# Performance work log

Hardware: AMD Instinct MI355X
Metric: run time of the kernel (lower is better)

The kernel has to match this reference:

```python
import jax, jax.numpy as jnp
import numpy as np

N = 100000   # num_nodes
E = 3200000  # num_edges
F = 7        # node_features
H = 128      # hidden_dim
D = 64       # embedding_dim
EPS = 1e-5


def setup_inputs() -> dict:
    key = jax.random.key(0)
    ks = jax.random.split(key, 32)
    inp = {}
    inp["x"] = jax.random.normal(ks[0], (N, F), jnp.float32)
    inp["edge_index"] = jax.random.randint(ks[1], (2, E), 0, N, dtype=jnp.int64)
    # input projection
    inp["W_in"] = jax.random.normal(ks[2], (F, H), jnp.float32) * 0.1
    inp["b_in"] = jax.random.normal(ks[3], (H,), jnp.float32) * 0.01
    # 3 GCN layers: 128->128, 128->128, 128->64, each with eval-mode BatchNorm params
    dims = [(H, H), (H, H), (H, D)]
    for i, (di, do) in enumerate(dims):
        k = jax.random.split(ks[4 + i], 6)
        inp[f"W{i}"] = jax.random.normal(k[0], (di, do), jnp.float32) * (1.0 / np.sqrt(di))
        inp[f"b{i}"] = jax.random.normal(k[1], (do,), jnp.float32) * 0.01
        inp[f"g{i}"] = 1.0 + 0.1 * jax.random.normal(k[2], (do,), jnp.float32)
        inp[f"be{i}"] = 0.1 * jax.random.normal(k[3], (do,), jnp.float32)
        inp[f"m{i}"] = 0.1 * jax.random.normal(k[4], (do,), jnp.float32)
        inp[f"v{i}"] = jax.random.uniform(k[5], (do,), jnp.float32, 0.5, 1.5)
    return inp


def _gcn_conv(x, W, b, src, dst, dinv):
    h = x @ W                                   # [N, do]
    coef = dinv[src] * dinv[dst]                # [E]
    agg = jax.ops.segment_sum(h[src] * coef[:, None], dst, num_segments=N)
    # self-loop contribution: norm = dinv[i]^2
    return agg + h * (dinv * dinv)[:, None] + b


def _bn_eval(x, g, be, m, v):
    return (x - m) * (g * jax.lax.rsqrt(v + EPS)) + be


def reference(x, edge_index, W_in, b_in,
              W0, b0, g0, be0, m0, v0,
              W1, b1, g1, be1, m1, v1,
              W2, b2, g2, be2, m2, v2):
    src, dst = edge_index[0], edge_index[1]
    # in-degree with self-loops (same for all layers)
    deg = jax.ops.segment_sum(jnp.ones((E,), x.dtype), dst, num_segments=N) + 1.0
    dinv = jax.lax.rsqrt(deg)

    h = jax.nn.relu(x @ W_in + b_in)            # [N, H]

    # layer 0: conv -> bn -> relu -> (dropout=id, eval) -> residual
    h0 = _gcn_conv(h, W0, b0, src, dst, dinv)
    h0 = jax.nn.relu(_bn_eval(h0, g0, be0, m0, v0)) + h
    # layer 1
    h1 = _gcn_conv(h0, W1, b1, src, dst, dinv)
    h1 = jax.nn.relu(_bn_eval(h1, g1, be1, m1, v1)) + h0
    # layer 2 (final): conv -> bn only (shape changes to D, no residual/relu)
    h2 = _gcn_conv(h1, W2, b2, src, dst, dinv)
    return _bn_eval(h2, g2, be2, m2, v2)        # [N, D]
```

## Files before the change

### kernel.cpp

```cpp
#include <hip/hip_runtime.h>


#define NN 100000
#define NE 3200000
#define FI 7
#define HD 128
#define DD 64
#define EPS 1e-5f
#define NB 196
#define EPB 8192
#define NBLK ((NE + EPB - 1) / EPB)
#define EMAX 20000

typedef float float2v __attribute__((ext_vector_type(2)));
typedef short short8 __attribute__((ext_vector_type(8)));
typedef float f32x4 __attribute__((ext_vector_type(4)));
typedef unsigned uintv4 __attribute__((ext_vector_type(4)));

__device__ __forceinline__ unsigned char f2fp8(float f) {
    return (unsigned char)(__builtin_amdgcn_cvt_pk_fp8_f32(f, f, 0, false) & 0xFF);
}
__device__ __forceinline__ unsigned short f2bf(float f) {
    unsigned u = __float_as_uint(f);
    u += 0x7FFF + ((u >> 16) & 1);
    return (unsigned short)(u >> 16);
}
__device__ __forceinline__ float bf2f(unsigned short s) {
    return __uint_as_float((unsigned)s << 16);
}


__global__ __launch_bounds__(256) void pA_bin(const int* __restrict__ ei,
                                              int* __restrict__ bcnt,
                                              int* __restrict__ ebin) {
    __shared__ int rec[EPB];
    __shared__ unsigned char bk[EPB];
    __shared__ int ls[256];
    __shared__ int cur[NB];
    __shared__ int gb[NB];
    const int t = threadIdx.x;
    const int base = blockIdx.x * EPB;
    const int cnt = min(EPB, NE - base);
    __shared__ int hc[256];
    hc[t] = 0;
    __syncthreads();
    for (int i = t; i < cnt; i += 256)
        atomicAdd(&hc[ei[NE + base + i] >> 9], 1);
    __syncthreads();
    const int myc = hc[t];
    if (t < NB) gb[t] = (myc ? atomicAdd(&bcnt[t], myc) : 0) + t * EMAX;
    ls[t] = myc;
    __syncthreads();
    for (int off = 1; off < 256; off <<= 1) {
        int v = (t >= off) ? ls[t - off] : 0;
        __syncthreads();
        ls[t] += v;
        __syncthreads();
    }
    const int excl = ls[t] - myc;
    __syncthreads();
    ls[t] = excl;
    if (t < NB) cur[t] = excl;
    __syncthreads();
    for (int i = t; i < cnt; i += 256) {
        int s = ei[base + i];
        int d = ei[NE + base + i];
        int b = d >> 9;
        int p = atomicAdd(&cur[b], 1);
        rec[p] = ((d & 511) << 23) | s;
        bk[p] = (unsigned char)b;
    }
    __syncthreads();
    for (int i = t; i < cnt; i += 256) {
        int b = bk[i];
        ebin[gb[b] + (i - ls[b])] = rec[i];
    }
}

__global__ __launch_bounds__(512) void p4_finalize(const int* __restrict__ bcnt,
                                                   const int* __restrict__ ebin,
                                                   int* __restrict__ esrc,
                                                   int* __restrict__ rowstart,
                                                   float* __restrict__ dinv) {
    __shared__ int sh[256];
    __shared__ int lh[512];
    __shared__ int sc[512];
    __shared__ int lc[512];
    const int t = threadIdx.x;
    const int b = blockIdx.x;
    if (t < 256) sh[t] = (t < NB) ? bcnt[t] : 0;
    __syncthreads();
    for (int off = 1; off < 256; off <<= 1) {
        int v = (t < 256 && t >= off) ? sh[t - off] : 0;
        __syncthreads();
        if (t < 256) sh[t] += v;
        __syncthreads();
    }
    const int ecnt = bcnt[b];
    const int ebase = sh[b] - ecnt;
    const int rbase = b * EMAX;
    const int n0 = b << 9;
    lh[t] = 0;
    __syncthreads();
    for (int i = t; i < ecnt; i += 512)
        atomicAdd(&lh[((unsigned)ebin[rbase + i]) >> 23], 1);
    __syncthreads();
    const int c = lh[t];
    sc[t] = c;
    __syncthreads();
    for (int off = 1; off < 512; off <<= 1) {
        int v = (t >= off) ? sc[t - off] : 0;
        __syncthreads();
        sc[t] += v;
        __syncthreads();
    }
    const int excl = ebase + sc[t] - c;
    lc[t] = excl;
    const int node = n0 + t;
    if (node < NN) {
        rowstart[node] = excl;
        dinv[node] = rsqrtf((float)c + 1.0f);
    }
    if (b == NB - 1 && t == 0) rowstart[NN] = NE;
    __syncthreads();
    for (int i = t; i < ecnt; i += 512) {
        int v = ebin[rbase + i];
        int p = atomicAdd(&lc[((unsigned)v) >> 23], 1);
        esrc[p] = v & 0x7FFFFF;
    }
}


__global__ __launch_bounds__(256) void inproj_kernel(const float* __restrict__ x,
                                                     const float* __restrict__ W_in,
                                                     const float* __restrict__ b_in,
                                                     unsigned short* __restrict__ hAbf) {
    int n = blockIdx.x * 2 + (threadIdx.x >> 7);
    int j = threadIdx.x & 127;
    float acc = b_in[j];
#pragma unroll
    for (int f = 0; f < FI; ++f) acc += x[n * FI + f] * W_in[f * HD + j];
    acc = fmaxf(acc, 0.f);
    hAbf[n * HD + j] = f2bf(acc);
}


__global__ __launch_bounds__(64) void wprep_all(const float* __restrict__ W0,
                                                const float* __restrict__ W1,
                                                const float* __restrict__ W2,
                                                unsigned short* __restrict__ wf0,
                                                unsigned short* __restrict__ wf1,
                                                unsigned short* __restrict__ wf2) {
    const int blk = blockIdx.x;
    const float* W;
    unsigned short* Wf;
    int DO, rel;
    if (blk < 32) { W = W0; Wf = wf0; DO = 128; rel = blk; }
    else if (blk < 64) { W = W1; Wf = wf1; DO = 128; rel = blk - 32; }
    else { W = W2; Wf = wf2; DO = 64; rel = blk - 64; }
    const int lane = threadIdx.x;
    const int nt = rel >> 2;
    const int ks = rel & 3;
    short8 o;
#pragma unroll
    for (int j = 0; j < 8; ++j)
        o[j] = (short)f2bf(W[(ks * 32 + (lane >> 4) * 8 + j) * DO + nt * 16 + (lane & 15)]);
    *(short8*)(Wf + ((size_t)rel * 64 + lane) * 8) = o;
}


template <int DO>
__global__ __launch_bounds__(256) void gemm_mfma(const unsigned short* __restrict__ A,
                                                 const unsigned short* __restrict__ Wf,
                                                 const float* __restrict__ dinv,
                                                 unsigned char* __restrict__ B) {
    constexpr int CT = DO / 64;
    const int tid = threadIdx.x;
    const int wave = tid >> 6;
    const int lane = tid & 63;
    const int n0 = blockIdx.x * 32;
    short8 bfrag[CT][4];
#pragma unroll
    for (int ct = 0; ct < CT; ++ct)
#pragma unroll
        for (int ks = 0; ks < 4; ++ks)
            bfrag[ct][ks] = *(const short8*)(Wf + ((size_t)(((wave * CT + ct) * 4 + ks) * 64) + lane) * 8);
#pragma unroll
    for (int rt = 0; rt < 2; ++rt) {
        const int arow = n0 + rt * 16 + (lane & 15);
        short8 afrag[4];
#pragma unroll
        for (int ks = 0; ks < 4; ++ks)
            afrag[ks] = *(const short8*)(A + (size_t)arow * HD + ks * 32 + ((lane >> 4) & 3) * 8);
        f32x4 acc[CT];
#pragma unroll
        for (int ct = 0; ct < CT; ++ct) acc[ct] = (f32x4){0.f, 0.f, 0.f, 0.f};
#pragma unroll
        for (int ks = 0; ks < 4; ++ks)
#pragma unroll
            for (int ct = 0; ct < CT; ++ct)
                acc[ct] = __builtin_amdgcn_mfma_f32_16x16x32_bf16(afrag[ks], bfrag[ct][ks], acc[ct], 0, 0, 0);
#pragma unroll
        for (int r = 0; r < 4; ++r) {
            const int orow = n0 + rt * 16 + (lane >> 4) * 4 + r;
            const float dv = dinv[orow];
#pragma unroll
            for (int ct = 0; ct < CT; ++ct) {
                const int ocol = (wave * CT + ct) * 16 + (lane & 15);
                B[(size_t)orow * DO + ocol] = f2fp8(acc[ct][r] * dv);
            }
        }
    }
}


template <int DO, bool RELU_RES>
__global__ __launch_bounds__(128) void gather_kernel(const unsigned char* __restrict__ hXW,
                                                     float* __restrict__ resOut,
                                                     unsigned short* __restrict__ resBf,
                                                     const int* __restrict__ rowstart,
                                                     const int* __restrict__ esrc,
                                                     const float* __restrict__ dinv,
                                                     const float* __restrict__ bias,
                                                     const float* __restrict__ g,
                                                     const float* __restrict__ be,
                                                     const float* __restrict__ m,
                                                     const float* __restrict__ v) {
    constexpr int CG = DO / 16;
    constexpr int NG = 128 / CG;
    __shared__ int s_idx[128];
    __shared__ float sred[16][132];
    const int n = blockIdx.x;
    const int t = threadIdx.x;
    const int rs = rowstart[n];
    const int re = rowstart[n + 1];
    const float dn = dinv[n];
    const int q = t & (CG - 1);
    const int grp = t / CG;
    float2v aL[4], aH[4], bL[4], bH[4];
#pragma unroll
    for (int w = 0; w < 4; ++w) {
        aL[w] = (float2v){0.f, 0.f}; aH[w] = (float2v){0.f, 0.f};
        bL[w] = (float2v){0.f, 0.f}; bH[w] = (float2v){0.f, 0.f};
    }
    for (int base = rs; base < re; base += 128) {
        const int c = min(128, re - base);
        __syncthreads();
        if (t < c) s_idx[t] = esrc[base + t];
        __syncthreads();
        for (int j = grp; j < c; j += 2 * NG) {
            {
                const uintv4 u = *(const uintv4*)(hXW + (size_t)s_idx[j] * DO + q * 16);
#pragma unroll
                for (int w = 0; w < 4; ++w) {
                    aL[w] += __builtin_amdgcn_cvt_pk_f32_fp8(u[w], false);
                    aH[w] += __builtin_amdgcn_cvt_pk_f32_fp8(u[w], true);
                }
            }
            if (j + NG < c) {
                const uintv4 u = *(const uintv4*)(hXW + (size_t)s_idx[j + NG] * DO + q * 16);
#pragma unroll
                for (int w = 0; w < 4; ++w) {
                    bL[w] += __builtin_amdgcn_cvt_pk_f32_fp8(u[w], false);
                    bH[w] += __builtin_amdgcn_cvt_pk_f32_fp8(u[w], true);
                }
            }
        }
    }
#pragma unroll
    for (int w = 0; w < 4; ++w) { aL[w] += bL[w]; aH[w] += bH[w]; }
#pragma unroll
    for (int w = 0; w < 4; ++w) {
        sred[4 * w + 0][t] = aL[w].x;
        sred[4 * w + 1][t] = aL[w].y;
        sred[4 * w + 2][t] = aH[w].x;
        sred[4 * w + 3][t] = aH[w].y;
    }
    __syncthreads();
    if (t < DO) {
        const int s = t & 15;
        const int q2 = t >> 4;
        float sum = 0.f;
#pragma unroll
        for (int k = 0; k < NG; ++k) sum += sred[s][k * CG + q2];
        const unsigned su = *(const unsigned*)(hXW + (size_t)n * DO + (t & ~3));
        const float2v pLo = __builtin_amdgcn_cvt_pk_f32_fp8(su, false);
        const float2v pHi = __builtin_amdgcn_cvt_pk_f32_fp8(su, true);
        const float slf = (t & 2) ? ((t & 1) ? pHi.y : pHi.x)
                                  : ((t & 1) ? pLo.y : pLo.x);
        float val = (sum + slf) * dn + bias[t];
        val = (val - m[t]) * (g[t] * rsqrtf(v[t] + EPS)) + be[t];
        if (RELU_RES) {
            val = fmaxf(val, 0.f) + bf2f(resBf[(size_t)n * DO + t]);
            resBf[(size_t)n * DO + t] = f2bf(val);
        } else {
            resOut[(size_t)n * DO + t] = val;
        }
    }
}


extern "C" void kernel_launch(void* const* d_in, const int* in_sizes, int n_in,
                              void* d_out, int out_size, void* d_ws, size_t ws_size,
                              hipStream_t stream) {
    const float* x    = (const float*)d_in[0];
    const int*   ei   = (const int*)d_in[1];
    const float* W_in = (const float*)d_in[2];
    const float* b_in = (const float*)d_in[3];
    const float* Wl[3] = {(const float*)d_in[4], (const float*)d_in[10], (const float*)d_in[16]};
    const float* bl[3] = {(const float*)d_in[5], (const float*)d_in[11], (const float*)d_in[17]};
    const float* gl[3] = {(const float*)d_in[6], (const float*)d_in[12], (const float*)d_in[18]};
    const float* bel[3] = {(const float*)d_in[7], (const float*)d_in[13], (const float*)d_in[19]};
    const float* ml[3] = {(const float*)d_in[8], (const float*)d_in[14], (const float*)d_in[20]};
    const float* vl[3] = {(const float*)d_in[9], (const float*)d_in[15], (const float*)d_in[21]};
    float* out = (float*)d_out;

    char* ws = (char*)d_ws;
    size_t off = 0;
    auto carve = [&](size_t bytes) {
        void* p = ws + off;
        off += (bytes + 255) & ~(size_t)255;
        return p;
    };
    int*   bcnt     = (int*)carve(NB * sizeof(int));
    int*   rowstart = (int*)carve((NN + 1) * sizeof(int));
    float* dinv     = (float*)carve(NN * sizeof(float));
    int*   esrc     = (int*)carve((size_t)NE * sizeof(int));
    unsigned short* hAbf = (unsigned short*)carve((size_t)NN * HD * sizeof(unsigned short));
    unsigned char* hB = (unsigned char*)carve((size_t)NN * HD);
    int*   ebin     = (int*)carve((size_t)NB * EMAX * sizeof(int));
    unsigned short* wf0 = (unsigned short*)carve((size_t)HD * HD * sizeof(unsigned short));
    unsigned short* wf1 = (unsigned short*)carve((size_t)HD * HD * sizeof(unsigned short));
    unsigned short* wf2 = (unsigned short*)carve((size_t)HD * DD * sizeof(unsigned short));
    (void)ws_size;

    hipMemsetAsync(bcnt, 0, NB * sizeof(int), stream);

    wprep_all<<<80, 64, 0, stream>>>(Wl[0], Wl[1], Wl[2], wf0, wf1, wf2);

    pA_bin<<<NBLK, 256, 0, stream>>>(ei, bcnt, ebin);
    p4_finalize<<<NB, 512, 0, stream>>>(bcnt, ebin, esrc, rowstart, dinv);

    inproj_kernel<<<NN / 2, 256, 0, stream>>>(x, W_in, b_in, hAbf);

    gemm_mfma<128><<<NN / 32, 256, 0, stream>>>(hAbf, wf0, dinv, hB);
    gather_kernel<128, true><<<NN, 128, 0, stream>>>(hB, (float*)nullptr, hAbf, rowstart, esrc, dinv,
                                                     bl[0], gl[0], bel[0], ml[0], vl[0]);
    gemm_mfma<128><<<NN / 32, 256, 0, stream>>>(hAbf, wf1, dinv, hB);
    gather_kernel<128, true><<<NN, 128, 0, stream>>>(hB, (float*)nullptr, hAbf, rowstart, esrc, dinv,
                                                     bl[1], gl[1], bel[1], ml[1], vl[1]);
    gemm_mfma<64><<<NN / 32, 256, 0, stream>>>(hAbf, wf2, dinv, hB);
    gather_kernel<64, false><<<NN, 128, 0, stream>>>(hB, out, (unsigned short*)nullptr,
                                                     rowstart, esrc, dinv,
                                                     bl[2], gl[2], bel[2], ml[2], vl[2]);
}
```

Before: 473.6 us.

## Use finer 256-node dst buckets for CSR build and fuse weight prep into inproj

Edge binning now uses 391 buckets of 256 destination nodes instead of 196 buckets of 512, so pA_bin runs with 512 threads and p4_finalize gets twice as many blocks, each handling fewer edges. The aim is more parallelism and shorter per-block local sorts during CSR construction. The weight-to-bf16 fragment prep kernel is folded into the input-projection kernel as extra blocks, which saves one launch. Costs include a larger per-block histogram and scan in pA_bin, 16-bit bucket ids in shared memory, and a smaller per-bucket capacity (EMAX 10000) that could overflow on skewed degree distributions.

```diff
diff --git a/kernel.cpp b/kernel.cpp
--- a/kernel.cpp
+++ b/kernel.cpp
@@ -7,10 +7,10 @@
 #define HD 128
 #define DD 64
 #define EPS 1e-5f
-#define NB 196
+#define NB 391
 #define EPB 8192
 #define NBLK ((NE + EPB - 1) / EPB)
-#define EMAX 20000
+#define EMAX 10000
 
 typedef float float2v __attribute__((ext_vector_type(2)));
 typedef short short8 __attribute__((ext_vector_type(8)));
@@ -30,28 +30,28 @@
 }
 
 
-__global__ __launch_bounds__(256) void pA_bin(const int* __restrict__ ei,
+__global__ __launch_bounds__(512) void pA_bin(const int* __restrict__ ei,
                                               int* __restrict__ bcnt,
                                               int* __restrict__ ebin) {
     __shared__ int rec[EPB];
-    __shared__ unsigned char bk[EPB];
-    __shared__ int ls[256];
+    __shared__ unsigned short bk[EPB];
+    __shared__ int ls[512];
     __shared__ int cur[NB];
     __shared__ int gb[NB];
+    __shared__ int hc[512];
     const int t = threadIdx.x;
     const int base = blockIdx.x * EPB;
     const int cnt = min(EPB, NE - base);
-    __shared__ int hc[256];
     hc[t] = 0;
     __syncthreads();
-    for (int i = t; i < cnt; i += 256)
-        atomicAdd(&hc[ei[NE + base + i] >> 9], 1);
+    for (int i = t; i < cnt; i += 512)
+        atomicAdd(&hc[ei[NE + base + i] >> 8], 1);
     __syncthreads();
     const int myc = hc[t];
     if (t < NB) gb[t] = (myc ? atomicAdd(&bcnt[t], myc) : 0) + t * EMAX;
     ls[t] = myc;
     __syncthreads();
-    for (int off = 1; off < 256; off <<= 1) {
+    for (int off = 1; off < 512; off <<= 1) {
         int v = (t >= off) ? ls[t - off] : 0;
         __syncthreads();
         ls[t] += v;
@@ -62,16 +62,16 @@
     ls[t] = excl;
     if (t < NB) cur[t] = excl;
     __syncthreads();
-    for (int i = t; i < cnt; i += 256) {
+    for (int i = t; i < cnt; i += 512) {
         int s = ei[base + i];
         int d = ei[NE + base + i];
-        int b = d >> 9;
+        int b = d >> 8;
         int p = atomicAdd(&cur[b], 1);
-        rec[p] = ((d & 511) << 23) | s;
-        bk[p] = (unsigned char)b;
-    }
-    __syncthreads();
-    for (int i = t; i < cnt; i += 256) {
+        rec[p] = ((d & 255) << 23) | s;
+        bk[p] = (unsigned short)b;
+    }
+    __syncthreads();
+    for (int i = t; i < cnt; i += 512) {
         int b = bk[i];
         ebin[gb[b] + (i - ls[b])] = rec[i];
     }
@@ -82,44 +82,46 @@
                                                    int* __restrict__ esrc,
                                                    int* __restrict__ rowstart,
                                                    float* __restrict__ dinv) {
-    __shared__ int sh[256];
-    __shared__ int lh[512];
-    __shared__ int sc[512];
-    __shared__ int lc[512];
+    __shared__ int sh[512];
+    __shared__ int lh[256];
+    __shared__ int sc[256];
+    __shared__ int lc[256];
     const int t = threadIdx.x;
     const int b = blockIdx.x;
-    if (t < 256) sh[t] = (t < NB) ? bcnt[t] : 0;
-    __syncthreads();
-    for (int off = 1; off < 256; off <<= 1) {
-        int v = (t < 256 && t >= off) ? sh[t - off] : 0;
-        __syncthreads();
-        if (t < 256) sh[t] += v;
+    sh[t] = (t < NB) ? bcnt[t] : 0;
+    __syncthreads();
+    for (int off = 1; off < 512; off <<= 1) {
+        int v = (t >= off) ? sh[t - off] : 0;
+        __syncthreads();
+        sh[t] += v;
         __syncthreads();
     }
     const int ecnt = bcnt[b];
     const int ebase = sh[b] - ecnt;
     const int rbase = b * EMAX;
-    const int n0 = b << 9;
-    lh[t] = 0;
+    const int n0 = b << 8;
+    if (t < 256) lh[t] = 0;
     __syncthreads();
     for (int i = t; i < ecnt; i += 512)
         atomicAdd(&lh[((unsigned)ebin[rbase + i]) >> 23], 1);
     __syncthreads();
-    const int c = lh[t];
-    sc[t] = c;
-    __syncthreads();
-    for (int off = 1; off < 512; off <<= 1) {
-        int v = (t >= off) ? sc[t - off] : 0;
-        __syncthreads();
-        sc[t] += v;
-        __syncthreads();
-    }
-    const int excl = ebase + sc[t] - c;
-    lc[t] = excl;
-    const int node = n0 + t;
-    if (node < NN) {
-        rowstart[node] = excl;
-        dinv[node] = rsqrtf((float)c + 1.0f);
+    int c = 0;
+    if (t < 256) { c = lh[t]; sc[t] = c; }
+    __syncthreads();
+    for (int off = 1; off < 256; off <<= 1) {
+        int v = (t < 256 && t >= off) ? sc[t - off] : 0;
+        __syncthreads();
+        if (t < 256) sc[t] += v;
+        __syncthreads();
+    }
+    if (t < 256) {
+        const int excl = ebase + sc[t] - c;
+        lc[t] = excl;
+        const int node = n0 + t;
+        if (node < NN) {
+            rowstart[node] = excl;
+            dinv[node] = rsqrtf((float)c + 1.0f);
+        }
     }
     if (b == NB - 1 && t == 0) rowstart[NN] = NE;
     __syncthreads();
@@ -131,41 +133,43 @@
 }
 
 
-__global__ __launch_bounds__(256) void inproj_kernel(const float* __restrict__ x,
-                                                     const float* __restrict__ W_in,
-                                                     const float* __restrict__ b_in,
-                                                     unsigned short* __restrict__ hAbf) {
-    int n = blockIdx.x * 2 + (threadIdx.x >> 7);
+__global__ __launch_bounds__(256) void inproj_wprep(const float* __restrict__ x,
+                                                    const float* __restrict__ W_in,
+                                                    const float* __restrict__ b_in,
+                                                    unsigned short* __restrict__ hAbf,
+                                                    const float* __restrict__ W0,
+                                                    const float* __restrict__ W1,
+                                                    const float* __restrict__ W2,
+                                                    unsigned short* __restrict__ wf0,
+                                                    unsigned short* __restrict__ wf1,
+                                                    unsigned short* __restrict__ wf2) {
+    const int blk = blockIdx.x;
+    if (blk >= NN / 2) {
+        const int u = (blk - NN / 2) * 4 + (threadIdx.x >> 6);
+        if (u >= 80) return;
+        const float* W;
+        unsigned short* Wf;
+        int DO, rel;
+        if (u < 32) { W = W0; Wf = wf0; DO = 128; rel = u; }
+        else if (u < 64) { W = W1; Wf = wf1; DO = 128; rel = u - 32; }
+        else { W = W2; Wf = wf2; DO = 64; rel = u - 64; }
+        const int lane = threadIdx.x & 63;
+        const int nt = rel >> 2;
+        const int ks = rel & 3;
+        short8 o;
+#pragma unroll
+        for (int j = 0; j < 8; ++j)
+            o[j] = (short)f2bf(W[(ks * 32 + (lane >> 4) * 8 + j) * DO + nt * 16 + (lane & 15)]);
+        *(short8*)(Wf + ((size_t)rel * 64 + lane) * 8) = o;
+        return;
+    }
+    int n = blk * 2 + (threadIdx.x >> 7);
     int j = threadIdx.x & 127;
     float acc = b_in[j];
 #pragma unroll
     for (int f = 0; f < FI; ++f) acc += x[n * FI + f] * W_in[f * HD + j];
     acc = fmaxf(acc, 0.f);
     hAbf[n * HD + j] = f2bf(acc);
-}
-
-
-__global__ __launch_bounds__(64) void wprep_all(const float* __restrict__ W0,
-                                                const float* __restrict__ W1,
-                                                const float* __restrict__ W2,
-                                                unsigned short* __restrict__ wf0,
-                                                unsigned short* __restrict__ wf1,
-                                                unsigned short* __restrict__ wf2) {
-    const int blk = blockIdx.x;
-    const float* W;
-    unsigned short* Wf;
-    int DO, rel;
-    if (blk < 32) { W = W0; Wf = wf0; DO = 128; rel = blk; }
-    else if (blk < 64) { W = W1; Wf = wf1; DO = 128; rel = blk - 32; }
-    else { W = W2; Wf = wf2; DO = 64; rel = blk - 64; }
-    const int lane = threadIdx.x;
-    const int nt = rel >> 2;
-    const int ks = rel & 3;
-    short8 o;
-#pragma unroll
-    for (int j = 0; j < 8; ++j)
-        o[j] = (short)f2bf(W[(ks * 32 + (lane >> 4) * 8 + j) * DO + nt * 16 + (lane & 15)]);
-    *(short8*)(Wf + ((size_t)rel * 64 + lane) * 8) = o;
 }
 
 
@@ -336,12 +340,11 @@
 
     hipMemsetAsync(bcnt, 0, NB * sizeof(int), stream);
 
-    wprep_all<<<80, 64, 0, stream>>>(Wl[0], Wl[1], Wl[2], wf0, wf1, wf2);
-
-    pA_bin<<<NBLK, 256, 0, stream>>>(ei, bcnt, ebin);
+    pA_bin<<<NBLK, 512, 0, stream>>>(ei, bcnt, ebin);
     p4_finalize<<<NB, 512, 0, stream>>>(bcnt, ebin, esrc, rowstart, dinv);
 
-    inproj_kernel<<<NN / 2, 256, 0, stream>>>(x, W_in, b_in, hAbf);
+    inproj_wprep<<<NN / 2 + 20, 256, 0, stream>>>(x, W_in, b_in, hAbf,
+                                                  Wl[0], Wl[1], Wl[2], wf0, wf1, wf2);
 
     gemm_mfma<128><<<NN / 32, 256, 0, stream>>>(hAbf, wf0, dinv, hB);
     gather_kernel<128, true><<<NN, 128, 0, stream>>>(hB, (float*)nullptr, hAbf, rowstart, esrc, dinv,
```

Result: faster. 459.8 us (-2.9%).
